# Kernel optimization log

Measured on AMD Instinct MI355X. Metric: run time of the kernel, lower is better.

The kernel has to match this reference:

```python
import jax, jax.numpy as jnp
import numpy as np

N = 50000      # num_nodes
R = 51         # num relations (after enrichment: inverse + self-loop)
E = 16         # emb_dim
C = 8          # num_classes
B = 40         # bases
NNZ = 1_600_000  # number of triples / nonzeros per adjacency


def setup_inputs() -> dict:
    key = jax.random.key(0)
    ks = jax.random.split(key, 7)
    # random triples (s, p, o)
    s = jax.random.randint(ks[0], (NNZ,), 0, N, dtype=jnp.int32)
    o = jax.random.randint(ks[1], (NNZ,), 0, N, dtype=jnp.int32)
    p = jax.random.randint(ks[2], (NNZ,), 0, R, dtype=jnp.int32)
    # horizontal adjacency: A_hor[s, p*N + o];  vertical: A_ver[p*N + s, o]
    hor_rows = s
    hor_cols = p * N + o
    ver_rows = p * N + s
    ver_cols = o
    # values = ones / row-sum of vertical graph (sum_sparse_rgcn normalization),
    # shared by hor and ver graphs as in the torch module
    deg = jax.ops.segment_sum(jnp.ones((NNZ,), jnp.float32), ver_rows,
                              num_segments=R * N)
    values = 1.0 / deg[ver_rows]
    # parameters (basis decomposition for both layers)
    comps1 = jax.random.normal(ks[3], (R, B), dtype=jnp.float32) * 0.05
    bases1 = jax.random.normal(ks[4], (B, N, E), dtype=jnp.float32) * 0.05
    comps2 = jax.random.normal(ks[5], (R, B), dtype=jnp.float32) * 0.05
    bases2 = jax.random.normal(ks[6], (B, E, C), dtype=jnp.float32) * 0.05
    bias1 = jnp.zeros((E,), jnp.float32)
    bias2 = jnp.zeros((C,), jnp.float32)
    return {
        'values': values, 'comps1': comps1, 'bases1': bases1,
        'comps2': comps2, 'bases2': bases2, 'bias1': bias1, 'bias2': bias2,
        'hor_rows': hor_rows, 'hor_cols': hor_cols,
        'ver_rows': ver_rows, 'ver_cols': ver_cols,
    }


def reference(values, comps1, bases1, comps2, bases2, bias1, bias2,
              hor_rows, hor_cols, ver_rows, ver_cols):
    b, n, e = bases1.shape
    r = comps1.shape[0]
    c = bases2.shape[2]
    # layer 1: basis-composed weights (r, n, e) -> flat (r*n, e)
    W1 = jnp.matmul(comps1, bases1.reshape(b, n * e)).reshape(r * n, e)
    # h = hor_graph @ W1   (sparse (n, r*n) x dense (r*n, e)) via gather+scatter
    h = jax.ops.segment_sum(values[:, None] * W1[hor_cols], hor_rows,
                            num_segments=n)          # (n, e)
    h = jax.nn.relu(h + bias1)
    # hv = ver_graph @ h   (sparse (r*n, n) x dense (n, e))
    hv = jax.ops.segment_sum(values[:, None] * h[ver_cols], ver_rows,
                             num_segments=r * n).reshape(r, n, e)
    # layer 2: basis-composed weights (r, e, c), bmm + sum over relations
    W2 = jnp.matmul(comps2, bases2.reshape(b, e * c)).reshape(r, e, c)
    out = jnp.einsum('rne,rec->nc', hv, W2) + bias2   # (n, c)
    return out
```

## Files before the change

### kernel.cpp

```cpp
#include <hip/hip_runtime.h>
#include <hip/hip_bf16.h>

constexpr int N   = 50000;
constexpr int R   = 51;
constexpr int E   = 16;
constexpr int C   = 8;
constexpr int B   = 40;
constexpr int NNZ = 1600000;

constexpr int BSH   = 6;
constexpr int BKN   = 1 << BSH;
constexpr int NB    = (N + BKN - 1) >> BSH;
constexpr int NBLK  = 784;
constexpr int CHUNK = (NNZ + NBLK - 1) / NBLK;

__global__ __launch_bounds__(256) void w1_gemm_kernel(
    const float* __restrict__ comps1, const float* __restrict__ bases1,
    float* __restrict__ W1) {
  constexpr int NC2 = N * E / 2;
  int j = blockIdx.x * blockDim.x + threadIdx.x;
  if (j >= NC2) return;
  const float2* b2 = reinterpret_cast<const float2*>(bases1);
  float2 col[B];
#pragma unroll
  for (int b = 0; b < B; ++b) col[b] = b2[b * NC2 + j];
  float2* w2p = reinterpret_cast<float2*>(W1);
#pragma unroll 1
  for (int r = 0; r < R; ++r) {
    float ax = 0.f, ay = 0.f;
#pragma unroll
    for (int b = 0; b < B; ++b) {
      float cc = comps1[r * B + b];
      ax = fmaf(cc, col[b].x, ax);
      ay = fmaf(cc, col[b].y, ay);
    }
    w2p[r * NC2 + j] = make_float2(ax, ay);
  }
}

__global__ __launch_bounds__(256) void count_kernel(
    const int* __restrict__ rows, int* __restrict__ gcount) {
  __shared__ int hist[NB];
  for (int i = threadIdx.x; i < NB; i += 256) hist[i] = 0;
  __syncthreads();
  int lo = blockIdx.x * CHUNK;
  int hi = lo + CHUNK < NNZ ? lo + CHUNK : NNZ;
  for (int i = lo + threadIdx.x; i < hi; i += 256)
    atomicAdd(&hist[rows[i] >> BSH], 1);
  __syncthreads();
  for (int i = threadIdx.x; i < NB; i += 256)
    if (hist[i]) atomicAdd(&gcount[i], hist[i]);
}

__global__ __launch_bounds__(1024) void scan_kernel(
    const int* __restrict__ gcount, int* __restrict__ gstart,
    int* __restrict__ gcursor) {
  __shared__ int buf[1024];
  int t = threadIdx.x;
  int own = (t < NB) ? gcount[t] : 0;
  buf[t] = own;
  __syncthreads();
  for (int d = 1; d < 1024; d <<= 1) {
    int v = (t >= d) ? buf[t - d] : 0;
    __syncthreads();
    buf[t] += v;
    __syncthreads();
  }
  if (t < NB) {
    int st = buf[t] - own;
    gstart[t] = st;
    gcursor[t] = st;
  }
  if (t == NB - 1) gstart[NB] = buf[t];
}

__global__ __launch_bounds__(256) void scatter_kernel(
    const int* __restrict__ rows, const int* __restrict__ cols,
    const float* __restrict__ vals, int* __restrict__ gcursor,
    int2* __restrict__ packed) {
  __shared__ int hist[NB];
  __shared__ int base[NB];
  for (int i = threadIdx.x; i < NB; i += 256) hist[i] = 0;
  __syncthreads();
  int lo = blockIdx.x * CHUNK;
  int hi = lo + CHUNK < NNZ ? lo + CHUNK : NNZ;
  for (int i = lo + threadIdx.x; i < hi; i += 256)
    atomicAdd(&hist[rows[i] >> BSH], 1);
  __syncthreads();
  for (int i = threadIdx.x; i < NB; i += 256) {
    int c = hist[i];
    base[i] = c ? atomicAdd(&gcursor[i], c) : 0;
  }
  __syncthreads();
  for (int i = threadIdx.x; i < NB; i += 256) hist[i] = 0;
  __syncthreads();
  for (int i = lo + threadIdx.x; i < hi; i += 256) {
    int s = rows[i];
    int b = s >> BSH;
    int pos = base[b] + atomicAdd(&hist[b], 1);
    packed[pos] = make_int2(((s & (BKN - 1)) << 26) | cols[i],
                            __float_as_int(vals[i]));
  }
}

__global__ void w2_gemm_kernel(const float* __restrict__ comps2,
                               const float* __restrict__ bases2,
                               float* __restrict__ W2g) {
  int i = blockIdx.x * blockDim.x + threadIdx.x;
  if (i >= R * E * C) return;
  int r = i >> 7;
  int ec = i & 127;
  float acc = 0.f;
#pragma unroll
  for (int b = 0; b < B; ++b)
    acc = fmaf(comps2[r * B + b], bases2[b * 128 + ec], acc);
  W2g[i] = acc;
}

__global__ __launch_bounds__(256) void layer1_kernel(
    const float* __restrict__ W1, const int* __restrict__ gstart,
    const int2* __restrict__ packed, const float* __restrict__ bias1,
    float* __restrict__ h) {
  __shared__ float hacc[BKN * 17];
  for (int i = threadIdx.x; i < BKN * 17; i += 256) hacc[i] = 0.f;
  __syncthreads();
  int bkt = blockIdx.x;
  int lo = gstart[bkt], hi = gstart[bkt + 1];
  const float4* W14 = reinterpret_cast<const float4*>(W1);
  for (int e = lo + threadIdx.x; e < hi; e += 256) {
    int2 pk = packed[e];
    int slo = ((unsigned)pk.x) >> 26;
    int col = pk.x & ((1 << 26) - 1);
    float v = __int_as_float(pk.y);
    float4 w0 = W14[col * 4 + 0];
    float4 w1 = W14[col * 4 + 1];
    float4 w2 = W14[col * 4 + 2];
    float4 w3 = W14[col * 4 + 3];
    float* hp = &hacc[slo * 17];
    atomicAdd(hp + 0,  v * w0.x);
    atomicAdd(hp + 1,  v * w0.y);
    atomicAdd(hp + 2,  v * w0.z);
    atomicAdd(hp + 3,  v * w0.w);
    atomicAdd(hp + 4,  v * w1.x);
    atomicAdd(hp + 5,  v * w1.y);
    atomicAdd(hp + 6,  v * w1.z);
    atomicAdd(hp + 7,  v * w1.w);
    atomicAdd(hp + 8,  v * w2.x);
    atomicAdd(hp + 9,  v * w2.y);
    atomicAdd(hp + 10, v * w2.z);
    atomicAdd(hp + 11, v * w2.w);
    atomicAdd(hp + 12, v * w3.x);
    atomicAdd(hp + 13, v * w3.y);
    atomicAdd(hp + 14, v * w3.z);
    atomicAdd(hp + 15, v * w3.w);
  }
  __syncthreads();
  for (int i = threadIdx.x; i < BKN * E; i += 256) {
    int slo = i >> 4, e = i & 15;
    int node = (bkt << BSH) + slo;
    if (node < N)
      h[node * E + e] = fmaxf(hacc[slo * 17 + e] + bias1[e], 0.f);
  }
}

__global__ __launch_bounds__(256) void layer2_kernel(
    const float* __restrict__ h, const float* __restrict__ W2g,
    const int* __restrict__ gstart, const int2* __restrict__ packed,
    const float* __restrict__ bias2, float* __restrict__ out) {
  __shared__ float w2s[R * 132];
  __shared__ float oacc[BKN * 9];
  for (int i = threadIdx.x; i < R * E * C; i += 256) {
    int p = i >> 7, ec = i & 127;
    int e = ec >> 3, c = ec & 7;
    w2s[p * 132 + c * 16 + e] = W2g[i];
  }
  for (int i = threadIdx.x; i < BKN * 9; i += 256) oacc[i] = 0.f;
  __syncthreads();
  int bkt = blockIdx.x;
  int lo = gstart[bkt], hi = gstart[bkt + 1];
  const float4* H4 = reinterpret_cast<const float4*>(h);
  for (int idx = lo + threadIdx.x; idx < hi; idx += 256) {
    int2 pk = packed[idx];
    int slo = ((unsigned)pk.x) >> 26;
    int col = pk.x & ((1 << 26) - 1);
    float v = __int_as_float(pk.y);
    int p = (int)((unsigned)col / (unsigned)N);
    int o = col - p * N;
    float4 h0 = H4[o * 4 + 0];
    float4 h1 = H4[o * 4 + 1];
    float4 h2 = H4[o * 4 + 2];
    float4 h3 = H4[o * 4 + 3];
    const float4* wp = reinterpret_cast<const float4*>(&w2s[p * 132]);
#pragma unroll
    for (int c = 0; c < 8; ++c) {
      float4 a = wp[c * 4 + 0];
      float4 bq = wp[c * 4 + 1];
      float4 cq = wp[c * 4 + 2];
      float4 dq = wp[c * 4 + 3];
      float s = h0.x * a.x + h0.y * a.y + h0.z * a.z + h0.w * a.w
              + h1.x * bq.x + h1.y * bq.y + h1.z * bq.z + h1.w * bq.w
              + h2.x * cq.x + h2.y * cq.y + h2.z * cq.z + h2.w * cq.w
              + h3.x * dq.x + h3.y * dq.y + h3.z * dq.z + h3.w * dq.w;
      atomicAdd(&oacc[slo * 9 + c], v * s);
    }
  }
  __syncthreads();
  for (int i = threadIdx.x; i < BKN * C; i += 256) {
    int slo = i >> 3, c = i & 7;
    int node = (bkt << BSH) + slo;
    if (node < N) out[node * C + c] = oacc[slo * 9 + c] + bias2[c];
  }
}

extern "C" void kernel_launch(void* const* d_in, const int* in_sizes, int n_in,
                              void* d_out, int out_size, void* d_ws, size_t ws_size,
                              hipStream_t stream) {
  const float* values  = (const float*)d_in[0];
  const float* comps1  = (const float*)d_in[1];
  const float* bases1  = (const float*)d_in[2];
  const float* comps2  = (const float*)d_in[3];
  const float* bases2  = (const float*)d_in[4];
  const float* bias1   = (const float*)d_in[5];
  const float* bias2   = (const float*)d_in[6];
  const int* hor_rows  = (const int*)d_in[7];
  const int* hor_cols  = (const int*)d_in[8];
  float* out = (float*)d_out;

  char* ws = (char*)d_ws;
  size_t off = 0;
  auto alloc = [&](size_t bytes) {
    void* p = ws + off;
    off += (bytes + 255) & ~size_t(255);
    return p;
  };
  float* W1     = (float*)alloc((size_t)R * N * E * 4);
  float* h      = (float*)alloc((size_t)N * E * 4);
  float* W2g    = (float*)alloc((size_t)R * E * C * 4);
  int*   gcount = (int*)alloc((size_t)NB * 4);
  int*   gstart = (int*)alloc((size_t)(NB + 1) * 4);
  int*   gcursor= (int*)alloc((size_t)NB * 4);
  int2*  packed = (int2*)alloc((size_t)NNZ * 8);
  (void)ws_size; (void)in_sizes; (void)n_in; (void)out_size;

  hipMemsetAsync(gcount, 0, (size_t)NB * 4, stream);

  w1_gemm_kernel<<<(N * E / 2 + 255) / 256, 256, 0, stream>>>(comps1, bases1, W1);
  count_kernel<<<NBLK, 256, 0, stream>>>(hor_rows, gcount);
  scan_kernel<<<1, 1024, 0, stream>>>(gcount, gstart, gcursor);
  scatter_kernel<<<NBLK, 256, 0, stream>>>(hor_rows, hor_cols, values, gcursor,
                                           packed);
  w2_gemm_kernel<<<(R * E * C + 255) / 256, 256, 0, stream>>>(comps2, bases2, W2g);
  layer1_kernel<<<NB, 256, 0, stream>>>(W1, gstart, packed, bias1, h);
  layer2_kernel<<<NB, 256, 0, stream>>>(h, W2g, gstart, packed, bias2, out);
}
```

Baseline: 622.0 us.

## Store W1 in bf16, split each bucket across four blocks, add reduction kernels

W1 is now stored as packed bf16 pairs, which halves the write traffic of the large basis-composed weight matrix and the gather traffic in layer 1. Layer 1 and layer 2 each split every row bucket across four blocks that write partial sums. New relu and out kernels add the partials, apply the bias, and apply relu where needed, which raises parallelism from 782 blocks. The scatter kernel's block count changes and the W1 GEMM moves later in the launch order. This risks bf16 rounding error in W1 and adds extra partial-buffer traffic and launches.

```diff
diff --git a/kernel.cpp b/kernel.cpp
--- a/kernel.cpp
+++ b/kernel.cpp
@@ -8,23 +8,27 @@
 constexpr int B   = 40;
 constexpr int NNZ = 1600000;
 
-constexpr int BSH   = 6;
-constexpr int BKN   = 1 << BSH;
-constexpr int NB    = (N + BKN - 1) >> BSH;
-constexpr int NBLK  = 784;
-constexpr int CHUNK = (NNZ + NBLK - 1) / NBLK;
+constexpr int BSH  = 6;
+constexpr int BKN  = 1 << BSH;
+constexpr int NB   = (N + BKN - 1) >> BSH;
+constexpr int NPAD = NB * BKN;
+constexpr int KS   = 4;
+
+constexpr int CBLK   = 784;
+constexpr int CCHUNK = (NNZ + CBLK - 1) / CBLK;
+constexpr int SBLK   = 256;
+constexpr int SCHUNK = (NNZ + SBLK - 1) / SBLK;
 
 __global__ __launch_bounds__(256) void w1_gemm_kernel(
     const float* __restrict__ comps1, const float* __restrict__ bases1,
-    float* __restrict__ W1) {
+    unsigned* __restrict__ W1u) {
   constexpr int NC2 = N * E / 2;
-  int j = blockIdx.x * blockDim.x + threadIdx.x;
+  int j = blockIdx.x * 256 + threadIdx.x;
   if (j >= NC2) return;
   const float2* b2 = reinterpret_cast<const float2*>(bases1);
   float2 col[B];
 #pragma unroll
   for (int b = 0; b < B; ++b) col[b] = b2[b * NC2 + j];
-  float2* w2p = reinterpret_cast<float2*>(W1);
 #pragma unroll 1
   for (int r = 0; r < R; ++r) {
     float ax = 0.f, ay = 0.f;
@@ -34,7 +38,9 @@
       ax = fmaf(cc, col[b].x, ax);
       ay = fmaf(cc, col[b].y, ay);
     }
-    w2p[r * NC2 + j] = make_float2(ax, ay);
+    unsigned lo = __bfloat16_as_ushort(__float2bfloat16(ax));
+    unsigned hi = __bfloat16_as_ushort(__float2bfloat16(ay));
+    W1u[r * NC2 + j] = (hi << 16) | lo;
   }
 }
 
@@ -43,8 +49,8 @@
   __shared__ int hist[NB];
   for (int i = threadIdx.x; i < NB; i += 256) hist[i] = 0;
   __syncthreads();
-  int lo = blockIdx.x * CHUNK;
-  int hi = lo + CHUNK < NNZ ? lo + CHUNK : NNZ;
+  int lo = blockIdx.x * CCHUNK;
+  int hi = lo + CCHUNK < NNZ ? lo + CCHUNK : NNZ;
   for (int i = lo + threadIdx.x; i < hi; i += 256)
     atomicAdd(&hist[rows[i] >> BSH], 1);
   __syncthreads();
@@ -82,8 +88,8 @@
   __shared__ int base[NB];
   for (int i = threadIdx.x; i < NB; i += 256) hist[i] = 0;
   __syncthreads();
-  int lo = blockIdx.x * CHUNK;
-  int hi = lo + CHUNK < NNZ ? lo + CHUNK : NNZ;
+  int lo = blockIdx.x * SCHUNK;
+  int hi = lo + SCHUNK < NNZ ? lo + SCHUNK : NNZ;
   for (int i = lo + threadIdx.x; i < hi; i += 256)
     atomicAdd(&hist[rows[i] >> BSH], 1);
   __syncthreads();
@@ -118,55 +124,69 @@
 }
 
 __global__ __launch_bounds__(256) void layer1_kernel(
-    const float* __restrict__ W1, const int* __restrict__ gstart,
-    const int2* __restrict__ packed, const float* __restrict__ bias1,
-    float* __restrict__ h) {
+    const unsigned* __restrict__ W1u, const int* __restrict__ gstart,
+    const int2* __restrict__ packed, float* __restrict__ hpart) {
   __shared__ float hacc[BKN * 17];
   for (int i = threadIdx.x; i < BKN * 17; i += 256) hacc[i] = 0.f;
   __syncthreads();
-  int bkt = blockIdx.x;
-  int lo = gstart[bkt], hi = gstart[bkt + 1];
-  const float4* W14 = reinterpret_cast<const float4*>(W1);
-  for (int e = lo + threadIdx.x; e < hi; e += 256) {
+  int bkt = blockIdx.x >> 2, part = blockIdx.x & (KS - 1);
+  int lo = gstart[bkt], len = gstart[bkt + 1] - lo;
+  int a = lo + ((len * part) >> 2), b = lo + ((len * (part + 1)) >> 2);
+  const uint4* W14 = reinterpret_cast<const uint4*>(W1u);
+  for (int e = a + threadIdx.x; e < b; e += 256) {
     int2 pk = packed[e];
     int slo = ((unsigned)pk.x) >> 26;
     int col = pk.x & ((1 << 26) - 1);
     float v = __int_as_float(pk.y);
-    float4 w0 = W14[col * 4 + 0];
-    float4 w1 = W14[col * 4 + 1];
-    float4 w2 = W14[col * 4 + 2];
-    float4 w3 = W14[col * 4 + 3];
+    uint4 w0 = W14[col * 2 + 0];
+    uint4 w1 = W14[col * 2 + 1];
     float* hp = &hacc[slo * 17];
-    atomicAdd(hp + 0,  v * w0.x);
-    atomicAdd(hp + 1,  v * w0.y);
-    atomicAdd(hp + 2,  v * w0.z);
-    atomicAdd(hp + 3,  v * w0.w);
-    atomicAdd(hp + 4,  v * w1.x);
-    atomicAdd(hp + 5,  v * w1.y);
-    atomicAdd(hp + 6,  v * w1.z);
-    atomicAdd(hp + 7,  v * w1.w);
-    atomicAdd(hp + 8,  v * w2.x);
-    atomicAdd(hp + 9,  v * w2.y);
-    atomicAdd(hp + 10, v * w2.z);
-    atomicAdd(hp + 11, v * w2.w);
-    atomicAdd(hp + 12, v * w3.x);
-    atomicAdd(hp + 13, v * w3.y);
-    atomicAdd(hp + 14, v * w3.z);
-    atomicAdd(hp + 15, v * w3.w);
-  }
-  __syncthreads();
+    atomicAdd(hp + 0,  v * __uint_as_float(w0.x << 16));
+    atomicAdd(hp + 1,  v * __uint_as_float(w0.x & 0xffff0000u));
+    atomicAdd(hp + 2,  v * __uint_as_float(w0.y << 16));
+    atomicAdd(hp + 3,  v * __uint_as_float(w0.y & 0xffff0000u));
+    atomicAdd(hp + 4,  v * __uint_as_float(w0.z << 16));
+    atomicAdd(hp + 5,  v * __uint_as_float(w0.z & 0xffff0000u));
+    atomicAdd(hp + 6,  v * __uint_as_float(w0.w << 16));
+    atomicAdd(hp + 7,  v * __uint_as_float(w0.w & 0xffff0000u));
+    atomicAdd(hp + 8,  v * __uint_as_float(w1.x << 16));
+    atomicAdd(hp + 9,  v * __uint_as_float(w1.x & 0xffff0000u));
+    atomicAdd(hp + 10, v * __uint_as_float(w1.y << 16));
+    atomicAdd(hp + 11, v * __uint_as_float(w1.y & 0xffff0000u));
+    atomicAdd(hp + 12, v * __uint_as_float(w1.z << 16));
+    atomicAdd(hp + 13, v * __uint_as_float(w1.z & 0xffff0000u));
+    atomicAdd(hp + 14, v * __uint_as_float(w1.w << 16));
+    atomicAdd(hp + 15, v * __uint_as_float(w1.w & 0xffff0000u));
+  }
+  __syncthreads();
+  float* dst = hpart + (size_t)part * (NPAD * E) + ((size_t)bkt << BSH) * E;
   for (int i = threadIdx.x; i < BKN * E; i += 256) {
     int slo = i >> 4, e = i & 15;
-    int node = (bkt << BSH) + slo;
-    if (node < N)
-      h[node * E + e] = fmaxf(hacc[slo * 17 + e] + bias1[e], 0.f);
-  }
+    dst[i] = hacc[slo * 17 + e];
+  }
+}
+
+__global__ __launch_bounds__(256) void relu_kernel(
+    const float* __restrict__ hpart, const float* __restrict__ bias1,
+    float* __restrict__ h) {
+  int i = blockIdx.x * 256 + threadIdx.x;
+  if (i >= N * E / 4) return;
+  constexpr int P4 = NPAD * E / 4;
+  const float4* hp = reinterpret_cast<const float4*>(hpart);
+  float4 s0 = hp[i], s1 = hp[i + P4], s2 = hp[i + 2 * P4], s3 = hp[i + 3 * P4];
+  float4 bb = reinterpret_cast<const float4*>(bias1)[i & 3];
+  float4 r;
+  r.x = fmaxf(s0.x + s1.x + s2.x + s3.x + bb.x, 0.f);
+  r.y = fmaxf(s0.y + s1.y + s2.y + s3.y + bb.y, 0.f);
+  r.z = fmaxf(s0.z + s1.z + s2.z + s3.z + bb.z, 0.f);
+  r.w = fmaxf(s0.w + s1.w + s2.w + s3.w + bb.w, 0.f);
+  reinterpret_cast<float4*>(h)[i] = r;
 }
 
 __global__ __launch_bounds__(256) void layer2_kernel(
     const float* __restrict__ h, const float* __restrict__ W2g,
     const int* __restrict__ gstart, const int2* __restrict__ packed,
-    const float* __restrict__ bias2, float* __restrict__ out) {
+    float* __restrict__ opart) {
   __shared__ float w2s[R * 132];
   __shared__ float oacc[BKN * 9];
   for (int i = threadIdx.x; i < R * E * C; i += 256) {
@@ -176,10 +196,11 @@
   }
   for (int i = threadIdx.x; i < BKN * 9; i += 256) oacc[i] = 0.f;
   __syncthreads();
-  int bkt = blockIdx.x;
-  int lo = gstart[bkt], hi = gstart[bkt + 1];
+  int bkt = blockIdx.x >> 2, part = blockIdx.x & (KS - 1);
+  int lo = gstart[bkt], len = gstart[bkt + 1] - lo;
+  int a = lo + ((len * part) >> 2), b = lo + ((len * (part + 1)) >> 2);
   const float4* H4 = reinterpret_cast<const float4*>(h);
-  for (int idx = lo + threadIdx.x; idx < hi; idx += 256) {
+  for (int idx = a + threadIdx.x; idx < b; idx += 256) {
     int2 pk = packed[idx];
     int slo = ((unsigned)pk.x) >> 26;
     int col = pk.x & ((1 << 26) - 1);
@@ -193,11 +214,11 @@
     const float4* wp = reinterpret_cast<const float4*>(&w2s[p * 132]);
 #pragma unroll
     for (int c = 0; c < 8; ++c) {
-      float4 a = wp[c * 4 + 0];
+      float4 aq = wp[c * 4 + 0];
       float4 bq = wp[c * 4 + 1];
       float4 cq = wp[c * 4 + 2];
       float4 dq = wp[c * 4 + 3];
-      float s = h0.x * a.x + h0.y * a.y + h0.z * a.z + h0.w * a.w
+      float s = h0.x * aq.x + h0.y * aq.y + h0.z * aq.z + h0.w * aq.w
               + h1.x * bq.x + h1.y * bq.y + h1.z * bq.z + h1.w * bq.w
               + h2.x * cq.x + h2.y * cq.y + h2.z * cq.z + h2.w * cq.w
               + h3.x * dq.x + h3.y * dq.y + h3.z * dq.z + h3.w * dq.w;
@@ -205,11 +226,28 @@
     }
   }
   __syncthreads();
+  float* dst = opart + (size_t)part * (NPAD * C) + ((size_t)bkt << BSH) * C;
   for (int i = threadIdx.x; i < BKN * C; i += 256) {
     int slo = i >> 3, c = i & 7;
-    int node = (bkt << BSH) + slo;
-    if (node < N) out[node * C + c] = oacc[slo * 9 + c] + bias2[c];
-  }
+    dst[i] = oacc[slo * 9 + c];
+  }
+}
+
+__global__ __launch_bounds__(256) void out_kernel(
+    const float* __restrict__ opart, const float* __restrict__ bias2,
+    float* __restrict__ out) {
+  int i = blockIdx.x * 256 + threadIdx.x;
+  if (i >= N * C / 4) return;
+  constexpr int P4 = NPAD * C / 4;
+  const float4* op = reinterpret_cast<const float4*>(opart);
+  float4 s0 = op[i], s1 = op[i + P4], s2 = op[i + 2 * P4], s3 = op[i + 3 * P4];
+  float4 bb = reinterpret_cast<const float4*>(bias2)[i & 1];
+  float4 r;
+  r.x = s0.x + s1.x + s2.x + s3.x + bb.x;
+  r.y = s0.y + s1.y + s2.y + s3.y + bb.y;
+  r.z = s0.z + s1.z + s2.z + s3.z + bb.z;
+  r.w = s0.w + s1.w + s2.w + s3.w + bb.w;
+  reinterpret_cast<float4*>(out)[i] = r;
 }
 
 extern "C" void kernel_launch(void* const* d_in, const int* in_sizes, int n_in,
@@ -233,23 +271,27 @@
     off += (bytes + 255) & ~size_t(255);
     return p;
   };
-  float* W1     = (float*)alloc((size_t)R * N * E * 4);
-  float* h      = (float*)alloc((size_t)N * E * 4);
-  float* W2g    = (float*)alloc((size_t)R * E * C * 4);
-  int*   gcount = (int*)alloc((size_t)NB * 4);
-  int*   gstart = (int*)alloc((size_t)(NB + 1) * 4);
-  int*   gcursor= (int*)alloc((size_t)NB * 4);
-  int2*  packed = (int2*)alloc((size_t)NNZ * 8);
+  unsigned* W1u    = (unsigned*)alloc((size_t)R * N * E / 2 * 4);
+  float*    h      = (float*)alloc((size_t)N * E * 4);
+  float*    W2g    = (float*)alloc((size_t)R * E * C * 4);
+  int*      gcount = (int*)alloc((size_t)NB * 4);
+  int*      gstart = (int*)alloc((size_t)(NB + 1) * 4);
+  int*      gcursor= (int*)alloc((size_t)NB * 4);
+  int2*     packed = (int2*)alloc((size_t)NNZ * 8);
+  float*    hpart  = (float*)alloc((size_t)KS * NPAD * E * 4);
+  float*    opart  = (float*)alloc((size_t)KS * NPAD * C * 4);
   (void)ws_size; (void)in_sizes; (void)n_in; (void)out_size;
 
   hipMemsetAsync(gcount, 0, (size_t)NB * 4, stream);
 
-  w1_gemm_kernel<<<(N * E / 2 + 255) / 256, 256, 0, stream>>>(comps1, bases1, W1);
-  count_kernel<<<NBLK, 256, 0, stream>>>(hor_rows, gcount);
+  count_kernel<<<CBLK, 256, 0, stream>>>(hor_rows, gcount);
   scan_kernel<<<1, 1024, 0, stream>>>(gcount, gstart, gcursor);
-  scatter_kernel<<<NBLK, 256, 0, stream>>>(hor_rows, hor_cols, values, gcursor,
+  scatter_kernel<<<SBLK, 256, 0, stream>>>(hor_rows, hor_cols, values, gcursor,
                                            packed);
   w2_gemm_kernel<<<(R * E * C + 255) / 256, 256, 0, stream>>>(comps2, bases2, W2g);
-  layer1_kernel<<<NB, 256, 0, stream>>>(W1, gstart, packed, bias1, h);
-  layer2_kernel<<<NB, 256, 0, stream>>>(h, W2g, gstart, packed, bias2, out);
-}
+  w1_gemm_kernel<<<(N * E / 2 + 255) / 256, 256, 0, stream>>>(comps1, bases1, W1u);
+  layer1_kernel<<<NB * KS, 256, 0, stream>>>(W1u, gstart, packed, hpart);
+  relu_kernel<<<(N * E / 4 + 255) / 256, 256, 0, stream>>>(hpart, bias1, h);
+  layer2_kernel<<<NB * KS, 256, 0, stream>>>(h, W2g, gstart, packed, opart);
+  out_kernel<<<(N * C / 4 + 255) / 256, 256, 0, stream>>>(opart, bias2, out);
+}
```

Result: faster. 567.7 us (-8.7%).
